# Performance work log

Measured on AMD Instinct MI355X. Metric: run time of the kernel, lower is better.

The kernel has to match this reference:

```python
import jax, jax.numpy as jnp
import numpy as np

B, S, D = 2, 2048, 2048
H, G = 32, 8          # num_heads, num_kv_groups
GS = H // G           # group_size = 4
HD = D // H           # head_dim = 64


def setup_inputs() -> dict:
    key = jax.random.key(0)
    ks = jax.random.split(key, 5)
    x = jax.random.normal(ks[0], (B, S, D), dtype=jnp.float32)
    Wq = jax.random.normal(ks[1], (D, D), dtype=jnp.float32) * 0.02
    Wk = jax.random.normal(ks[2], (G * HD, D), dtype=jnp.float32) * 0.02
    Wv = jax.random.normal(ks[3], (G * HD, D), dtype=jnp.float32) * 0.02
    Wo = jax.random.normal(ks[4], (D, D), dtype=jnp.float32) * 0.02
    return {"x": x, "Wq": Wq, "Wk": Wk, "Wv": Wv, "Wo": Wo}


def reference(x, Wq, Wk, Wv, Wo):
    b, s, _ = x.shape
    # Projections (nn.Linear: x @ W.T, no bias)
    # queries: view(b,s,H,HD) with head h = g*GS + j -> reshape to (b,s,G,GS,HD)
    q = (x @ Wq.T).reshape(b, s, G, GS, HD)
    k = (x @ Wk.T).reshape(b, s, G, HD)   # [b, s, G, HD]
    v = (x @ Wv.T).reshape(b, s, G, HD)
    # repeat_interleave(group_size, dim=heads): head h uses kv group h // GS,
    # which is exactly the grouped einsum below (no materialized repeat).
    scores = jnp.einsum('bqgjd,bkgd->bgjqk', q, k) / np.sqrt(HD).astype(np.float32)
    # prefill cache: ptr=0, so mask is plain causal (q_pos < k_pos masked out)
    qpos = jnp.arange(s)
    mask = qpos[:, None] < qpos[None, :]        # [s, s], True = masked
    scores = jnp.where(mask, -jnp.inf, scores)
    w = jax.nn.softmax(scores, axis=-1)         # dropout p=0.0 (eval)
    ctx = jnp.einsum('bgjqk,bkgd->bqgjd', w, v).reshape(b, s, D)
    return ctx @ Wo.T
```

## Files before the change

kernel.cpp:

```cpp
#include <hip/hip_runtime.h>
#include <hip/hip_bf16.h>

typedef unsigned short u16;
typedef short bf16x4 __attribute__((ext_vector_type(4)));
typedef short bf16x8 __attribute__((ext_vector_type(8)));
typedef float f32x4 __attribute__((ext_vector_type(4)));

#define NEG_BIG (-1e30f)
#define SCL 0.18033688f

__device__ __forceinline__ u16 f2bf(float f) {
    union { float f; unsigned int u; } x; x.f = f;
    unsigned int r = x.u + 0x7fffu + ((x.u >> 16) & 1u);
    return (u16)(r >> 16);
}

__device__ __forceinline__ unsigned cvtpk(float lo, float hi) {
    unsigned r;
    asm("v_cvt_pk_bf16_f32 %0, %1, %2" : "=v"(r) : "v"(lo), "v"(hi));
    return r;
}

__device__ __forceinline__ f32x4 mfma16(bf16x4 a, bf16x4 b, f32x4 c) {
#if __has_builtin(__builtin_amdgcn_mfma_f32_16x16x16bf16_1k)
    return __builtin_amdgcn_mfma_f32_16x16x16bf16_1k(a, b, c, 0, 0, 0);
#else
    asm("v_mfma_f32_16x16x16_bf16 %0, %1, %2, %0" : "+v"(c) : "v"(a), "v"(b));
    return c;
#endif
}

__device__ __forceinline__ void dma16(const u16* g, const u16* lds) {
    __builtin_amdgcn_global_load_lds(
        (const __attribute__((address_space(1))) unsigned int*)g,
        (__attribute__((address_space(3))) unsigned int*)lds, 16, 0, 0);
}

__device__ __forceinline__ bf16x8 sfrag(const u16* lds, int row, int kb8) {
    int slot = row * 8 + (kb8 ^ (row & 7));
    return *(const bf16x8*)(lds + slot * 8);
}

__device__ __forceinline__ bf16x4 vfrag(const u16* lds, int row, int kb, int lhi) {
    int c = kb * 2 + (lhi >> 1);
    int slot = row * 8 + (c ^ (row & 7));
    return *(const bf16x4*)(lds + slot * 8 + (lhi & 1) * 4);
}

__global__ __launch_bounds__(256) void cvt_all(const float* __restrict__ x,
                                               const float* __restrict__ wq,
                                               const float* __restrict__ wk,
                                               const float* __restrict__ wv,
                                               const float* __restrict__ wo,
                                               u16* __restrict__ xb, u16* __restrict__ wqb,
                                               u16* __restrict__ wkb, u16* __restrict__ wvb,
                                               u16* __restrict__ wob) {
    size_t i = (size_t)blockIdx.x * 256 + threadIdx.x;
    const float* s; u16* d; size_t off;
    if      (i < 1048576) { s = x;  d = xb;  off = i; }
    else if (i < 1572864) { s = wq; d = wqb; off = i - 1048576; }
    else if (i < 1703936) { s = wk; d = wkb; off = i - 1572864; }
    else if (i < 1835008) { s = wv; d = wvb; off = i - 1703936; }
    else                  { s = wo; d = wob; off = i - 1835008; }
    const float* p = s + off * 8;
    float4 a = *(const float4*)p;
    float4 b = *(const float4*)(p + 4);
    bf16x8 r;
    r[0] = (short)f2bf(a.x); r[1] = (short)f2bf(a.y);
    r[2] = (short)f2bf(a.z); r[3] = (short)f2bf(a.w);
    r[4] = (short)f2bf(b.x); r[5] = (short)f2bf(b.y);
    r[6] = (short)f2bf(b.z); r[7] = (short)f2bf(b.w);
    *(bf16x8*)(d + off * 8) = r;
}

__global__ __launch_bounds__(256) void gemm_bt(const u16* __restrict__ A,
                                               const u16* __restrict__ Bt,
                                               float* __restrict__ C,
                                               int M, int N, int K) {
    __shared__ u16 As[8192];
    __shared__ u16 Bs[8192];
    const int t = threadIdx.x;
    const int wave = t >> 6, lane = t & 63;
    const int wm = (wave >> 1) * 64, wn = (wave & 1) * 64;
    const int lhi = lane >> 4, llo = lane & 15;
    const int m0 = blockIdx.y * 128, n0 = blockIdx.x * 128;
    const int wbase = wave * 64;

    f32x4 acc[4][4] = {};
    for (int k0 = 0; k0 < K; k0 += 64) {
        const u16* Ab = A + (size_t)m0 * K + k0;
        const u16* Bb = Bt + (size_t)n0 * K + k0;
#pragma unroll
        for (int i = 0; i < 4; ++i) {
            int s = i * 256 + t;
            int row = s >> 3, gch = (s & 7) ^ (row & 7);
            dma16(Ab + (size_t)row * K + gch * 8, As + (i * 256 + wbase) * 8);
            dma16(Bb + (size_t)row * K + gch * 8, Bs + (i * 256 + wbase) * 8);
        }
        __syncthreads();
#pragma unroll
        for (int ks = 0; ks < 2; ++ks) {
            const int kb = ks * 4 + lhi;
            bf16x8 af[4], bfg[4];
#pragma unroll
            for (int mi = 0; mi < 4; ++mi) af[mi] = sfrag(As, wm + mi * 16 + llo, kb);
#pragma unroll
            for (int ni = 0; ni < 4; ++ni) bfg[ni] = sfrag(Bs, wn + ni * 16 + llo, kb);
#pragma unroll
            for (int mi = 0; mi < 4; ++mi)
#pragma unroll
                for (int ni = 0; ni < 4; ++ni)
                    acc[mi][ni] = __builtin_amdgcn_mfma_f32_16x16x32_bf16(
                        af[mi], bfg[ni], acc[mi][ni], 0, 0, 0);
        }
        __syncthreads();
    }
#pragma unroll
    for (int mi = 0; mi < 4; ++mi)
#pragma unroll
        for (int ni = 0; ni < 4; ++ni)
#pragma unroll
            for (int r = 0; r < 4; ++r) {
                int row = m0 + wm + mi * 16 + lhi * 4 + r;
                int col = n0 + wn + ni * 16 + llo;
                C[(size_t)row * N + col] = acc[mi][ni][r];
            }
}

__global__ __launch_bounds__(256) void gemm_qkv(const u16* __restrict__ A,
                                                const u16* __restrict__ Wq,
                                                const u16* __restrict__ Wk,
                                                const u16* __restrict__ Wv,
                                                u16* __restrict__ Qout,
                                                u16* __restrict__ Kout,
                                                u16* __restrict__ Vtout) {
    const int K = 2048;
    __shared__ u16 As[8192];
    __shared__ u16 Bs[8192];
    const int t = threadIdx.x;
    const int wave = t >> 6, lane = t & 63;
    const int wm = (wave >> 1) * 64, wn = (wave & 1) * 64;
    const int lhi = lane >> 4, llo = lane & 15;
    const int m0 = blockIdx.y * 128;
    const int bx = blockIdx.x;
    const int kind = (bx < 16) ? 0 : (bx < 20 ? 1 : 2);
    const int n0 = (kind == 0) ? bx * 128 : (bx & 3) * 128;
    const u16* Bt = ((kind == 0) ? Wq : (kind == 1) ? Wk : Wv) + (size_t)n0 * K;
    const int wbase = wave * 64;

    f32x4 acc[4][4] = {};
    for (int k0 = 0; k0 < K; k0 += 64) {
        const u16* Ab = A + (size_t)m0 * K + k0;
        const u16* Bb = Bt + k0;
#pragma unroll
        for (int i = 0; i < 4; ++i) {
            int s = i * 256 + t;
            int row = s >> 3, gch = (s & 7) ^ (row & 7);
            dma16(Ab + (size_t)row * K + gch * 8, As + (i * 256 + wbase) * 8);
            dma16(Bb + (size_t)row * K + gch * 8, Bs + (i * 256 + wbase) * 8);
        }
        __syncthreads();
#pragma unroll
        for (int ks = 0; ks < 2; ++ks) {
            const int kb = ks * 4 + lhi;
            bf16x8 af[4], bfg[4];
#pragma unroll
            for (int mi = 0; mi < 4; ++mi) af[mi] = sfrag(As, wm + mi * 16 + llo, kb);
#pragma unroll
            for (int ni = 0; ni < 4; ++ni) bfg[ni] = sfrag(Bs, wn + ni * 16 + llo, kb);
#pragma unroll
            for (int mi = 0; mi < 4; ++mi)
#pragma unroll
                for (int ni = 0; ni < 4; ++ni)
                    acc[mi][ni] = __builtin_amdgcn_mfma_f32_16x16x32_bf16(
                        af[mi], bfg[ni], acc[mi][ni], 0, 0, 0);
        }
        __syncthreads();
    }

    if (kind == 0) {
#pragma unroll
        for (int mi = 0; mi < 4; ++mi)
#pragma unroll
            for (int ni = 0; ni < 4; ++ni)
#pragma unroll
                for (int r = 0; r < 4; ++r) {
                    int row = m0 + wm + mi * 16 + lhi * 4 + r;
                    int col = n0 + wn + ni * 16 + llo;
                    Qout[(size_t)row * 2048 + col] = f2bf(acc[mi][ni][r] * SCL);
                }
    } else if (kind == 1) {
#pragma unroll
        for (int mi = 0; mi < 4; ++mi)
#pragma unroll
            for (int ni = 0; ni < 4; ++ni)
#pragma unroll
                for (int r = 0; r < 4; ++r) {
                    int row = m0 + wm + mi * 16 + lhi * 4 + r;
                    int col = n0 + wn + ni * 16 + llo;
                    Kout[(size_t)row * 512 + col] = f2bf(acc[mi][ni][r]);
                }
    } else {
#pragma unroll
        for (int mi = 0; mi < 4; ++mi)
#pragma unroll
            for (int ni = 0; ni < 4; ++ni) {
                int row = m0 + wm + mi * 16 + lhi * 4;
                int col = n0 + wn + ni * 16 + llo;
                size_t off = ((size_t)col + (size_t)(row >> 11) * 512) * 2048 + (row & 2047);
                short4 v;
                v.x = (short)f2bf(acc[mi][ni][0]);
                v.y = (short)f2bf(acc[mi][ni][1]);
                v.z = (short)f2bf(acc[mi][ni][2]);
                v.w = (short)f2bf(acc[mi][ni][3]);
                *(short4*)(Vtout + off) = v;
            }
    }
}

__global__ __launch_bounds__(256, 4) void attn6(const u16* __restrict__ Q,
                                                const u16* __restrict__ Kbuf,
                                                const u16* __restrict__ Vtb,
                                                u16* __restrict__ Ctx) {
    __shared__ u16 Ks[2][4096];
    __shared__ u16 Vs[2][4096];
    const int bg = blockIdx.y;
    const int b = bg >> 3, g = bg & 7;
    const int t = threadIdx.x, w = t >> 6, lane = t & 63;
    const int lhi = lane >> 4, llo = lane & 15;
    const int h = g * 4 + w;
    const int wbase = w * 64;

    const u16* Kp = Kbuf + (size_t)(b * 2048) * 512 + g * 64;
    const u16* Vp = Vtb + (size_t)bg * 64 * 2048;

    const int r0 = t >> 3,          g0 = (t & 7) ^ (r0 & 7);
    const int r1 = (256 + t) >> 3,  g1 = ((256 + t) & 7) ^ (r1 & 7);

    bf16x4 ones;
    ones[0] = ones[1] = ones[2] = ones[3] = (short)0x3F80;

    auto STAGE = [&](int kt, int bufi) {
        const u16* Kt = Kp + (size_t)kt * 64 * 512;
        const u16* Vt2 = Vp + kt * 64;
        u16* Kd = Ks[bufi]; u16* Vd = Vs[bufi];
        dma16(Kt + (size_t)r0 * 512 + g0 * 8, Kd + wbase * 8);
        dma16(Vt2 + (size_t)r0 * 2048 + g0 * 8, Vd + wbase * 8);
        dma16(Kt + (size_t)r1 * 512 + g1 * 8, Kd + (256 + wbase) * 8);
        dma16(Vt2 + (size_t)r1 * 2048 + g1 * 8, Vd + (256 + wbase) * 8);
    };

#pragma unroll
    for (int ph = 0; ph < 2; ++ph) {
        const int qt = ph ? (int)blockIdx.x : 127 - (int)blockIdx.x;

        const u16* Qp = Q + ((size_t)(b * 2048 + qt * 16)) * 2048 + h * 64;
        bf16x8 aq[2];
#pragma unroll
        for (int ks = 0; ks < 2; ++ks)
            aq[ks] = *(const bf16x8*)(Qp + (size_t)llo * 2048 + ks * 32 + lhi * 8);

        f32x4 o[4] = {};
        f32x4 lac = {};
        float m_ = NEG_BIG;

        const int ktmax = (qt * 16 + 15) >> 6;

        STAGE(0, 0);
        asm volatile("s_waitcnt vmcnt(0)" ::: "memory");
        __builtin_amdgcn_s_barrier();

        for (int kt = 0; kt <= ktmax; ++kt) {
            const int cur = kt & 1;
            if (kt < ktmax) STAGE(kt + 1, cur ^ 1);
            const u16* Ksb = Ks[cur];
            const u16* Vsb = Vs[cur];

            f32x4 st[4] = {};
            __builtin_amdgcn_s_setprio(1);
#pragma unroll
            for (int ks = 0; ks < 2; ++ks) {
                const int kb8 = ks * 4 + lhi;
                bf16x8 kf[4];
#pragma unroll
                for (int kb = 0; kb < 4; ++kb) kf[kb] = sfrag(Ksb, kb * 16 + llo, kb8);
#pragma unroll
                for (int kb = 0; kb < 4; ++kb)
                    st[kb] = __builtin_amdgcn_mfma_f32_16x16x32_bf16(
                        kf[kb], aq[ks], st[kb], 0, 0, 0);
            }
            __builtin_amdgcn_s_setprio(0);

            if (kt * 64 + 63 > qt * 16) {
                int qg = qt * 16 + llo;
#pragma unroll
                for (int kb = 0; kb < 4; ++kb)
#pragma unroll
                    for (int r = 0; r < 4; ++r) {
                        int kg = kt * 64 + kb * 16 + lhi * 4 + r;
                        if (kg > qg) st[kb][r] = NEG_BIG;
                    }
            }

            float t0 = fmaxf(fmaxf(st[0][0], st[0][1]), st[0][2]);
            float t1 = fmaxf(fmaxf(st[0][3], st[1][0]), st[1][1]);
            float t2 = fmaxf(fmaxf(st[1][2], st[1][3]), st[2][0]);
            float t3 = fmaxf(fmaxf(st[2][1], st[2][2]), st[2][3]);
            float t4 = fmaxf(fmaxf(st[3][0], st[3][1]), st[3][2]);
            float mx = fmaxf(fmaxf(fmaxf(t0, t1), t2),
                             fmaxf(fmaxf(t3, t4), st[3][3]));
            mx = fmaxf(mx, __shfl_xor(mx, 16, 64));
            mx = fmaxf(mx, __shfl_xor(mx, 32, 64));

            if (__any(mx > m_ + 8.0f)) {
                float mn = fmaxf(m_, mx);
                float alpha = exp2f(m_ - mn);
                m_ = mn;
#pragma unroll
                for (int hb = 0; hb < 4; ++hb) o[hb] *= alpha;
                lac *= alpha;
            }

            bf16x4 pf[4];
#pragma unroll
            for (int kb = 0; kb < 4; ++kb) {
                float p0 = exp2f(st[kb][0] - m_);
                float p1 = exp2f(st[kb][1] - m_);
                float p2 = exp2f(st[kb][2] - m_);
                float p3 = exp2f(st[kb][3] - m_);
                union { unsigned u[2]; bf16x4 v; } pu;
                pu.u[0] = cvtpk(p0, p1);
                pu.u[1] = cvtpk(p2, p3);
                pf[kb] = pu.v;
            }

            __builtin_amdgcn_s_setprio(1);
#pragma unroll
            for (int kb = 0; kb < 4; ++kb) lac = mfma16(ones, pf[kb], lac);
#pragma unroll
            for (int kb = 0; kb < 4; ++kb)
#pragma unroll
                for (int hb = 0; hb < 4; ++hb)
                    o[hb] = mfma16(vfrag(Vsb, hb * 16 + llo, kb, lhi), pf[kb], o[hb]);
            __builtin_amdgcn_s_setprio(0);

            asm volatile("s_waitcnt vmcnt(0)" ::: "memory");
            __builtin_amdgcn_s_barrier();
        }

        float inv = 1.0f / lac[0];
        u16* Cp = Ctx + (size_t)(b * 2048 + qt * 16) * 2048 + h * 64;
#pragma unroll
        for (int hb = 0; hb < 4; ++hb) {
            union { unsigned u[2]; short4 s; } cu;
            cu.u[0] = cvtpk(o[hb][0] * inv, o[hb][1] * inv);
            cu.u[1] = cvtpk(o[hb][2] * inv, o[hb][3] * inv);
            *(short4*)(Cp + (size_t)llo * 2048 + hb * 16 + lhi * 4) = cu.s;
        }
    }
}

extern "C" void kernel_launch(void* const* d_in, const int* in_sizes, int n_in,
                              void* d_out, int out_size, void* d_ws, size_t ws_size,
                              hipStream_t stream) {
    const float* x  = (const float*)d_in[0];
    const float* Wq = (const float*)d_in[1];
    const float* Wk = (const float*)d_in[2];
    const float* Wv = (const float*)d_in[3];
    const float* Wo = (const float*)d_in[4];

    u16* xb  = (u16*)d_ws;
    u16* wqb = xb + 8388608;
    u16* wkb = wqb + 4194304;
    u16* wvb = wkb + 1048576;
    u16* wob = wvb + 1048576;
    u16* Kb  = wob + 4194304;
    u16* Vtb = Kb + 2097152;
    u16* Ctx = xb;
    u16* Qb  = (u16*)d_out;
    float* out = (float*)d_out;

    cvt_all<<<dim3(9216), 256, 0, stream>>>(x, Wq, Wk, Wv, Wo, xb, wqb, wkb, wvb, wob);
    gemm_qkv<<<dim3(24, 32), 256, 0, stream>>>(xb, wqb, wkb, wvb, Qb, Kb, Vtb);
    attn6<<<dim3(64, 16), 256, 0, stream>>>(Qb, Kb, Vtb, Ctx);
    gemm_bt<<<dim3(16, 32), 256, 0, stream>>>(Ctx, wob, out, 4096, 2048, 2048);
}
```

Baseline: 307.9 us.

## Triple-buffer GEMM loads with 512-thread 128x256 tiles and swizzled block order

```diff
diff --git a/kernel.cpp b/kernel.cpp
--- a/kernel.cpp
+++ b/kernel.cpp
@@ -73,47 +73,81 @@
     *(bf16x8*)(d + off * 8) = r;
 }
 
-__global__ __launch_bounds__(256) void gemm_bt(const u16* __restrict__ A,
-                                               const u16* __restrict__ Bt,
-                                               float* __restrict__ C,
-                                               int M, int N, int K) {
-    __shared__ u16 As[8192];
-    __shared__ u16 Bs[8192];
+
+__global__ __launch_bounds__(512, 2) void gemm_bt2(const u16* __restrict__ A,
+                                                   const u16* __restrict__ Bt,
+                                                   float* __restrict__ C) {
+    const int K = 2048, NT = 32;
+    __shared__ u16 SA[3][8192];
+    __shared__ u16 SB[3][16384];
     const int t = threadIdx.x;
-    const int wave = t >> 6, lane = t & 63;
-    const int wm = (wave >> 1) * 64, wn = (wave & 1) * 64;
+    const int w = t >> 6, lane = t & 63;
+    const int wr = w >> 2, wc = w & 3;
     const int lhi = lane >> 4, llo = lane & 15;
-    const int m0 = blockIdx.y * 128, n0 = blockIdx.x * 128;
-    const int wbase = wave * 64;
+    const int bid = (int)blockIdx.x;
+    const int lin = (bid & 7) * 32 + (bid >> 3);
+    const int by = lin & 31, bxN = lin >> 5;
+    const int m0 = by * 128, n0 = bxN * 256;
+
+    const u16* Abase = A + (size_t)m0 * K;
+    const u16* Bbase = Bt + (size_t)n0 * K;
+
+    auto STAGE = [&](int kt, int bufi) {
+        const u16* Ab = Abase + kt * 64;
+        const u16* Bb = Bbase + kt * 64;
+        const u16* Ad = SA[bufi];
+        const u16* Bd = SB[bufi];
+#pragma unroll
+        for (int i = 0; i < 2; ++i) {
+            int s = i * 512 + t;
+            int row = s >> 3, gch = (s & 7) ^ (row & 7);
+            dma16(Ab + (size_t)row * K + gch * 8, Ad + (i * 512 + w * 64) * 8);
+        }
+#pragma unroll
+        for (int i = 0; i < 4; ++i) {
+            int s = i * 512 + t;
+            int row = s >> 3, gch = (s & 7) ^ (row & 7);
+            dma16(Bb + (size_t)row * K + gch * 8, Bd + (i * 512 + w * 64) * 8);
+        }
+    };
 
     f32x4 acc[4][4] = {};
-    for (int k0 = 0; k0 < K; k0 += 64) {
-        const u16* Ab = A + (size_t)m0 * K + k0;
-        const u16* Bb = Bt + (size_t)n0 * K + k0;
-#pragma unroll
-        for (int i = 0; i < 4; ++i) {
-            int s = i * 256 + t;
-            int row = s >> 3, gch = (s & 7) ^ (row & 7);
-            dma16(Ab + (size_t)row * K + gch * 8, As + (i * 256 + wbase) * 8);
-            dma16(Bb + (size_t)row * K + gch * 8, Bs + (i * 256 + wbase) * 8);
-        }
-        __syncthreads();
+    STAGE(0, 0);
+    STAGE(1, 1);
+    int cur = 0;
+    for (int kt = 0; kt < NT; ++kt) {
+        __builtin_amdgcn_s_barrier();
+        if (kt + 2 < NT) {
+            int nb = cur + 2; if (nb >= 3) nb -= 3;
+            STAGE(kt + 2, nb);
+            asm volatile("s_waitcnt vmcnt(12)" ::: "memory");
+        } else if (kt + 1 < NT) {
+            asm volatile("s_waitcnt vmcnt(6)" ::: "memory");
+        } else {
+            asm volatile("s_waitcnt vmcnt(0)" ::: "memory");
+        }
+        __builtin_amdgcn_s_barrier();
+        __builtin_amdgcn_sched_barrier(0);
+        const u16* Ab = SA[cur];
+        const u16* Bb = SB[cur];
 #pragma unroll
         for (int ks = 0; ks < 2; ++ks) {
             const int kb = ks * 4 + lhi;
             bf16x8 af[4], bfg[4];
 #pragma unroll
-            for (int mi = 0; mi < 4; ++mi) af[mi] = sfrag(As, wm + mi * 16 + llo, kb);
-#pragma unroll
-            for (int ni = 0; ni < 4; ++ni) bfg[ni] = sfrag(Bs, wn + ni * 16 + llo, kb);
+            for (int mi = 0; mi < 4; ++mi) af[mi] = sfrag(Ab, wr * 64 + mi * 16 + llo, kb);
+#pragma unroll
+            for (int ni = 0; ni < 4; ++ni) bfg[ni] = sfrag(Bb, wc * 64 + ni * 16 + llo, kb);
+            __builtin_amdgcn_s_setprio(1);
 #pragma unroll
             for (int mi = 0; mi < 4; ++mi)
 #pragma unroll
                 for (int ni = 0; ni < 4; ++ni)
                     acc[mi][ni] = __builtin_amdgcn_mfma_f32_16x16x32_bf16(
                         af[mi], bfg[ni], acc[mi][ni], 0, 0, 0);
-        }
-        __syncthreads();
+            __builtin_amdgcn_s_setprio(0);
+        }
+        cur = cur + 1; if (cur >= 3) cur -= 3;
     }
 #pragma unroll
     for (int mi = 0; mi < 4; ++mi)
@@ -121,61 +155,92 @@
         for (int ni = 0; ni < 4; ++ni)
 #pragma unroll
             for (int r = 0; r < 4; ++r) {
-                int row = m0 + wm + mi * 16 + lhi * 4 + r;
-                int col = n0 + wn + ni * 16 + llo;
-                C[(size_t)row * N + col] = acc[mi][ni][r];
-            }
-}
-
-__global__ __launch_bounds__(256) void gemm_qkv(const u16* __restrict__ A,
-                                                const u16* __restrict__ Wq,
-                                                const u16* __restrict__ Wk,
-                                                const u16* __restrict__ Wv,
-                                                u16* __restrict__ Qout,
-                                                u16* __restrict__ Kout,
-                                                u16* __restrict__ Vtout) {
-    const int K = 2048;
-    __shared__ u16 As[8192];
-    __shared__ u16 Bs[8192];
+                int row = m0 + wr * 64 + mi * 16 + lhi * 4 + r;
+                int col = n0 + wc * 64 + ni * 16 + llo;
+                C[(size_t)row * 2048 + col] = acc[mi][ni][r];
+            }
+}
+
+__global__ __launch_bounds__(512, 2) void gemm_qkv2(const u16* __restrict__ A,
+                                                    const u16* __restrict__ Wq,
+                                                    const u16* __restrict__ Wk,
+                                                    const u16* __restrict__ Wv,
+                                                    u16* __restrict__ Qout,
+                                                    u16* __restrict__ Kout,
+                                                    u16* __restrict__ Vtout) {
+    const int K = 2048, NT = 32;
+    __shared__ u16 SA[3][8192];
+    __shared__ u16 SB[3][16384];
     const int t = threadIdx.x;
-    const int wave = t >> 6, lane = t & 63;
-    const int wm = (wave >> 1) * 64, wn = (wave & 1) * 64;
+    const int w = t >> 6, lane = t & 63;
+    const int wr = w >> 2, wc = w & 3;
     const int lhi = lane >> 4, llo = lane & 15;
-    const int m0 = blockIdx.y * 128;
-    const int bx = blockIdx.x;
-    const int kind = (bx < 16) ? 0 : (bx < 20 ? 1 : 2);
-    const int n0 = (kind == 0) ? bx * 128 : (bx & 3) * 128;
+    const int bid = (int)blockIdx.x;
+    const int lin = (bid & 7) * 48 + (bid >> 3);
+    const int by = lin & 31, bxN = lin >> 5;
+    const int m0 = by * 128;
+    const int kind = (bxN < 8) ? 0 : (bxN < 10 ? 1 : 2);
+    const int n0 = (kind == 0) ? bxN * 256 : (bxN & 1) * 256;
     const u16* Bt = ((kind == 0) ? Wq : (kind == 1) ? Wk : Wv) + (size_t)n0 * K;
-    const int wbase = wave * 64;
+
+    const u16* Abase = A + (size_t)m0 * K;
+
+    auto STAGE = [&](int kt, int bufi) {
+        const u16* Ab = Abase + kt * 64;
+        const u16* Bb = Bt + kt * 64;
+        const u16* Ad = SA[bufi];
+        const u16* Bd = SB[bufi];
+#pragma unroll
+        for (int i = 0; i < 2; ++i) {
+            int s = i * 512 + t;
+            int row = s >> 3, gch = (s & 7) ^ (row & 7);
+            dma16(Ab + (size_t)row * K + gch * 8, Ad + (i * 512 + w * 64) * 8);
+        }
+#pragma unroll
+        for (int i = 0; i < 4; ++i) {
+            int s = i * 512 + t;
+            int row = s >> 3, gch = (s & 7) ^ (row & 7);
+            dma16(Bb + (size_t)row * K + gch * 8, Bd + (i * 512 + w * 64) * 8);
+        }
+    };
 
     f32x4 acc[4][4] = {};
-    for (int k0 = 0; k0 < K; k0 += 64) {
-        const u16* Ab = A + (size_t)m0 * K + k0;
-        const u16* Bb = Bt + k0;
-#pragma unroll
-        for (int i = 0; i < 4; ++i) {
-            int s = i * 256 + t;
-            int row = s >> 3, gch = (s & 7) ^ (row & 7);
-            dma16(Ab + (size_t)row * K + gch * 8, As + (i * 256 + wbase) * 8);
-            dma16(Bb + (size_t)row * K + gch * 8, Bs + (i * 256 + wbase) * 8);
-        }
-        __syncthreads();
+    STAGE(0, 0);
+    STAGE(1, 1);
+    int cur = 0;
+    for (int kt = 0; kt < NT; ++kt) {
+        __builtin_amdgcn_s_barrier();
+        if (kt + 2 < NT) {
+            int nb = cur + 2; if (nb >= 3) nb -= 3;
+            STAGE(kt + 2, nb);
+            asm volatile("s_waitcnt vmcnt(12)" ::: "memory");
+        } else if (kt + 1 < NT) {
+            asm volatile("s_waitcnt vmcnt(6)" ::: "memory");
+        } else {
+            asm volatile("s_waitcnt vmcnt(0)" ::: "memory");
+        }
+        __builtin_amdgcn_s_barrier();
+        __builtin_amdgcn_sched_barrier(0);
+        const u16* Ab = SA[cur];
+        const u16* Bb = SB[cur];
 #pragma unroll
         for (int ks = 0; ks < 2; ++ks) {
             const int kb = ks * 4 + lhi;
             bf16x8 af[4], bfg[4];
 #pragma unroll
-            for (int mi = 0; mi < 4; ++mi) af[mi] = sfrag(As, wm + mi * 16 + llo, kb);
-#pragma unroll
-            for (int ni = 0; ni < 4; ++ni) bfg[ni] = sfrag(Bs, wn + ni * 16 + llo, kb);
+            for (int mi = 0; mi < 4; ++mi) af[mi] = sfrag(Ab, wr * 64 + mi * 16 + llo, kb);
+#pragma unroll
+            for (int ni = 0; ni < 4; ++ni) bfg[ni] = sfrag(Bb, wc * 64 + ni * 16 + llo, kb);
+            __builtin_amdgcn_s_setprio(1);
 #pragma unroll
             for (int mi = 0; mi < 4; ++mi)
 #pragma unroll
                 for (int ni = 0; ni < 4; ++ni)
                     acc[mi][ni] = __builtin_amdgcn_mfma_f32_16x16x32_bf16(
                         af[mi], bfg[ni], acc[mi][ni], 0, 0, 0);
-        }
-        __syncthreads();
+            __builtin_amdgcn_s_setprio(0);
+        }
+        cur = cur + 1; if (cur >= 3) cur -= 3;
     }
 
     if (kind == 0) {
@@ -185,8 +250,8 @@
             for (int ni = 0; ni < 4; ++ni)
 #pragma unroll
                 for (int r = 0; r < 4; ++r) {
-                    int row = m0 + wm + mi * 16 + lhi * 4 + r;
-                    int col = n0 + wn + ni * 16 + llo;
+                    int row = m0 + wr * 64 + mi * 16 + lhi * 4 + r;
+                    int col = n0 + wc * 64 + ni * 16 + llo;
                     Qout[(size_t)row * 2048 + col] = f2bf(acc[mi][ni][r] * SCL);
                 }
     } else if (kind == 1) {
@@ -196,8 +261,8 @@
             for (int ni = 0; ni < 4; ++ni)
 #pragma unroll
                 for (int r = 0; r < 4; ++r) {
-                    int row = m0 + wm + mi * 16 + lhi * 4 + r;
-                    int col = n0 + wn + ni * 16 + llo;
+                    int row = m0 + wr * 64 + mi * 16 + lhi * 4 + r;
+                    int col = n0 + wc * 64 + ni * 16 + llo;
                     Kout[(size_t)row * 512 + col] = f2bf(acc[mi][ni][r]);
                 }
     } else {
@@ -205,8 +270,8 @@
         for (int mi = 0; mi < 4; ++mi)
 #pragma unroll
             for (int ni = 0; ni < 4; ++ni) {
-                int row = m0 + wm + mi * 16 + lhi * 4;
-                int col = n0 + wn + ni * 16 + llo;
+                int row = m0 + wr * 64 + mi * 16 + lhi * 4;
+                int col = n0 + wc * 64 + ni * 16 + llo;
                 size_t off = ((size_t)col + (size_t)(row >> 11) * 512) * 2048 + (row & 2047);
                 short4 v;
                 v.x = (short)f2bf(acc[mi][ni][0]);
@@ -381,7 +446,7 @@
     float* out = (float*)d_out;
 
     cvt_all<<<dim3(9216), 256, 0, stream>>>(x, Wq, Wk, Wv, Wo, xb, wqb, wkb, wvb, wob);
-    gemm_qkv<<<dim3(24, 32), 256, 0, stream>>>(xb, wqb, wkb, wvb, Qb, Kb, Vtb);
+    gemm_qkv2<<<dim3(384), 512, 0, stream>>>(xb, wqb, wkb, wvb, Qb, Kb, Vtb);
     attn6<<<dim3(64, 16), 256, 0, stream>>>(Qb, Kb, Vtb, Ctx);
-    gemm_bt<<<dim3(16, 32), 256, 0, stream>>>(Ctx, wob, out, 4096, 2048, 2048);
-}
+    gemm_bt2<<<dim3(256), 512, 0, stream>>>(Ctx, wob, out);
+}
```

New measurement: 332.0 us. 7.8% more time.
